# Kernel tuning notes

Measured on AMD Instinct MI355X. Metric: run time of the kernel, lower is better.

Reference implementation:

```python
import jax, jax.numpy as jnp
import numpy as np

B, S, D, H = 2, 1024, 1024, 16
DK = D // H
NEG = -1000000000.0


def setup_inputs() -> dict:
    key = jax.random.key(0)
    ks = jax.random.split(key, 12)
    def lin(kw, kb):
        # torch nn.Linear default init: U(-1/sqrt(D), 1/sqrt(D))
        bound = 1.0 / np.sqrt(D)
        W = jax.random.uniform(kw, (D, D), jnp.float32, -bound, bound)
        b = jax.random.uniform(kb, (D,), jnp.float32, -bound, bound)
        return W, b
    Wq, bq = lin(ks[0], ks[1])
    Wk, bk = lin(ks[2], ks[3])
    Wv, bv = lin(ks[4], ks[5])
    Wo, bo = lin(ks[6], ks[7])
    q = jax.random.normal(ks[8], (B, S, D), jnp.float32)
    k = jax.random.normal(ks[9], (B, S, D), jnp.float32)
    v = jax.random.normal(ks[10], (B, S, D), jnp.float32)
    mask = jnp.ones((B, 1, S), jnp.int32)  # key-padding mask, 1 = keep
    return {"q": q, "k": k, "v": v, "mask": mask,
            "Wq": Wq, "bq": bq, "Wk": Wk, "bk": bk,
            "Wv": Wv, "bv": bv, "Wo": Wo, "bo": bo}


def reference(q, k, v, mask, Wq, bq, Wk, bk, Wv, bv, Wo, bo):
    b = q.shape[0]
    # projections -> [B, H, S, DK]
    def split_heads(x):
        return x.reshape(b, -1, H, DK).transpose(0, 2, 1, 3)
    qh = split_heads(q @ Wq.T + bq)
    kh = split_heads(k @ Wk.T + bk)
    vh = split_heads(v @ Wv.T + bv)
    # scores [B, H, S, S]
    scores = jnp.einsum('bhqd,bhkd->bhqk', qh, kh) / jnp.sqrt(jnp.float32(DK))
    m = mask[:, None]  # [B,1,1,S] broadcast over heads and query dim
    scores = jnp.where(m == 0, NEG, scores)
    attn = jax.nn.softmax(scores, axis=-1)  # dropout p=0.0 -> identity
    out = jnp.einsum('bhqk,bhkd->bhqd', attn, vh)
    concat = out.transpose(0, 2, 1, 3).reshape(b, -1, D)
    return concat @ Wo.T + bo
```

## Files before the change

### kernel.cpp

```cpp
#include <hip/hip_runtime.h>

#define H 16
#define DK 64
#define SD 1024
#define DD 1024
#define BB 2
#define MROWS (BB * SD)
#define KDIM 1024

typedef __attribute__((ext_vector_type(8))) short short8;
typedef __attribute__((ext_vector_type(4))) float floatx4;
typedef unsigned short u16;
typedef __attribute__((ext_vector_type(4))) unsigned short u16x4;

#if __has_builtin(__builtin_amdgcn_exp2f)
#define EXP2(x) __builtin_amdgcn_exp2f(x)
#else
#define EXP2(x) exp2f(x)
#endif
#if __has_builtin(__builtin_amdgcn_rcpf)
#define RCP(x) __builtin_amdgcn_rcpf(x)
#else
#define RCP(x) (1.0f / (x))
#endif

__device__ __forceinline__ u16 f2bf(float f) {
    union { float f; unsigned u; } v; v.f = f;
    unsigned u = v.u;
    return (u16)((u + 0x7FFFu + ((u >> 16) & 1u)) >> 16);
}

__device__ __forceinline__ void gload16(const void* g, void* l) {
    __builtin_amdgcn_global_load_lds((const __attribute__((address_space(1))) unsigned int*)g,
                                     (__attribute__((address_space(3))) unsigned int*)l, 16, 0, 0);
}

__global__ void cvt_all(const float4* __restrict__ q, const float4* __restrict__ k,
                        const float4* __restrict__ v, const float4* __restrict__ Wq,
                        const float4* __restrict__ Wk, const float4* __restrict__ Wv,
                        const float4* __restrict__ Wo, const int* __restrict__ mask,
                        u16x4* __restrict__ qb, u16x4* __restrict__ kb, u16x4* __restrict__ vb,
                        u16x4* __restrict__ Wqb, u16x4* __restrict__ Wkb, u16x4* __restrict__ Wvb,
                        u16x4* __restrict__ Wob, float* __restrict__ maskadd) {
    const int z = blockIdx.y;
    if (z == 7) {
        const int i = blockIdx.x * blockDim.x + threadIdx.x;
        if (i < BB * SD) maskadd[i] = (mask[i] != 0) ? 0.f : -1e9f;
        return;
    }
    const float4* src; u16x4* dst; int n4;
    switch (z) {
        case 0: src = q;  dst = qb;  n4 = MROWS * DD / 4; break;
        case 1: src = k;  dst = kb;  n4 = MROWS * DD / 4; break;
        case 2: src = v;  dst = vb;  n4 = MROWS * DD / 4; break;
        case 3: src = Wq; dst = Wqb; n4 = DD * DD / 4; break;
        case 4: src = Wk; dst = Wkb; n4 = DD * DD / 4; break;
        case 5: src = Wv; dst = Wvb; n4 = DD * DD / 4; break;
        default: src = Wo; dst = Wob; n4 = DD * DD / 4; break;
    }
    for (int i = blockIdx.x * blockDim.x + threadIdx.x; i < n4; i += gridDim.x * blockDim.x) {
        float4 f = src[i];
        u16x4 o;
        o.x = f2bf(f.x); o.y = f2bf(f.y); o.z = f2bf(f.z); o.w = f2bf(f.w);
        dst[i] = o;
    }
}

__device__ __forceinline__ void gemm_main64(const u16* __restrict__ A, const u16* __restrict__ W,
                                            u16* As, u16* Bs, floatx4 (&acc)[2][4],
                                            int row0, int col0) {
    const int tid = threadIdx.x;
    const int w = tid >> 6, lane = tid & 63, lg = lane >> 4, lr = lane & 15;
    const int lrow = lane >> 3;
    const int lcol = (lane & 7) * 8;

    const u16* Abase = A + (row0 + lrow) * KDIM + lcol;
    const u16* Wbase = W + (col0 + lrow) * KDIM + lcol;

#pragma unroll
    for (int j = 0; j < 4; j++) {
        const int seg = j * 4 + w;
        gload16(Abase + seg * 8 * KDIM, As + seg * 512);
    }
#pragma unroll
    for (int j = 0; j < 2; j++) {
        const int seg = j * 4 + w;
        gload16(Wbase + seg * 8 * KDIM, Bs + seg * 512);
    }
    __syncthreads();

    int buf = 0;
    for (int k0 = 0; k0 < KDIM; k0 += 64) {
        if (k0 + 64 < KDIM) {
            const int nb = buf ^ 1;
#pragma unroll
            for (int j = 0; j < 4; j++) {
                const int seg = j * 4 + w;
                gload16(Abase + seg * 8 * KDIM + k0 + 64, As + nb * 8192 + seg * 512);
            }
#pragma unroll
            for (int j = 0; j < 2; j++) {
                const int seg = j * 4 + w;
                gload16(Wbase + seg * 8 * KDIM + k0 + 64, Bs + nb * 4096 + seg * 512);
            }
        }
        const u16* Asb = As + buf * 8192;
        const u16* Bsb = Bs + buf * 4096;
        short8 af[2][2], bf[4][2];
#pragma unroll
        for (int kk = 0; kk < 2; kk++) {
#pragma unroll
            for (int mi = 0; mi < 2; mi++)
                af[mi][kk] = *(const short8*)&Asb[(w * 32 + mi * 16 + lr) * 64 + kk * 32 + lg * 8];
#pragma unroll
            for (int ni = 0; ni < 4; ni++)
                bf[ni][kk] = *(const short8*)&Bsb[(ni * 16 + lr) * 64 + kk * 32 + lg * 8];
        }
#pragma unroll
        for (int kk = 0; kk < 2; kk++)
#pragma unroll
            for (int mi = 0; mi < 2; mi++)
#pragma unroll
                for (int ni = 0; ni < 4; ni++)
                    acc[mi][ni] = __builtin_amdgcn_mfma_f32_16x16x32_bf16(af[mi][kk], bf[ni][kk], acc[mi][ni], 0, 0, 0);
        __syncthreads();
        buf ^= 1;
    }
}

__global__ __launch_bounds__(256) void gemm_qkv(const u16* __restrict__ qb, const u16* __restrict__ kb,
                                                const u16* __restrict__ vb, const u16* __restrict__ Wqb,
                                                const u16* __restrict__ Wkb, const u16* __restrict__ Wvb,
                                                const float* __restrict__ bq, const float* __restrict__ bk,
                                                const float* __restrict__ bv,
                                                u16* __restrict__ Qh, u16* __restrict__ Kf, u16* __restrict__ Vf) {
    __shared__ u16 As[2 * 128 * 64];
    __shared__ u16 Bs[2 * 64 * 64];
    const int id = blockIdx.x;
    const int xcd = id & 7, j = id >> 3;
    const int z = j >> 5, r = j & 31;
    const int by = (xcd << 1) | (r >> 4), bx = r & 15;

    const u16 *A, *W; const float* bias; u16* out; float scale;
    if (z == 0)      { A = qb; W = Wqb; bias = bq; out = Qh; scale = 0.18033688011112042f; }
    else if (z == 1) { A = kb; W = Wkb; bias = bk; out = Kf; scale = 1.f; }
    else             { A = vb; W = Wvb; bias = bv; out = Vf; scale = 1.f; }

    const int row0 = by * 128, col0 = bx * 64;
    floatx4 acc[2][4] = {};
    gemm_main64(A, W, As, Bs, acc, row0, col0);

    const int tid = threadIdx.x;
    const int w = tid >> 6, lane = tid & 63, lg = lane >> 4, lr = lane & 15;
#pragma unroll
    for (int mi = 0; mi < 2; mi++)
#pragma unroll
        for (int ni = 0; ni < 4; ni++) {
            const int col = col0 + ni * 16 + lr;
            const float bv_ = bias[col];
            const int h = col >> 6, dk = col & 63;
#pragma unroll
            for (int rr = 0; rr < 4; rr++) {
                const int row = row0 + w * 32 + mi * 16 + lg * 4 + rr;
                const int b = row >> 10, s = row & 1023;
                const int bh = b * H + h;
                const float val = (acc[mi][ni][rr] + bv_) * scale;
                if (z == 0) {
                    out[(bh * SD + s) * DK + dk] = f2bf(val);
                } else if (z == 1) {
                    out[bh * 65536 + (s >> 4) * 1024 + (dk >> 5) * 512 +
                        ((dk >> 3) & 3) * 128 + (s & 15) * 8 + (dk & 7)] = f2bf(val);
                } else {
                    out[bh * 65536 + (s >> 6) * 4096 + ((dk >> 4) * 2 + ((s >> 5) & 1)) * 512 +
                        ((s >> 3) & 3) * 128 + (dk & 15) * 8 + (s & 7)] = f2bf(val);
                }
            }
        }
}

__global__ __launch_bounds__(256) void gemm_o(const u16* __restrict__ A, const u16* __restrict__ W,
                                              const float* __restrict__ bias, float* __restrict__ out) {
    const int id = blockIdx.x;
    const int xcd = id & 7, j = id >> 3;
    const int by = (xcd << 1) | (j >> 4), bx = j & 15;
    const int row0 = by * 128, col0 = bx * 64;
    const int tid = threadIdx.x;
    const int w = tid >> 6, lane = tid & 63, lg = lane >> 4, lr = lane & 15;

    const u16* Ar0 = A + (row0 + w * 32 + lr) * KDIM + lg * 8;
    const u16* Ar1 = A + (row0 + w * 32 + 16 + lr) * KDIM + lg * 8;
    const u16* Wr0 = W + (col0 + lr) * KDIM + lg * 8;
    const u16* Wr1 = W + (col0 + 16 + lr) * KDIM + lg * 8;
    const u16* Wr2 = W + (col0 + 32 + lr) * KDIM + lg * 8;
    const u16* Wr3 = W + (col0 + 48 + lr) * KDIM + lg * 8;

    floatx4 acc[2][4] = {};

#pragma unroll 2
    for (int k0 = 0; k0 < KDIM; k0 += 64) {
        short8 af[2][2], bf[4][2];
#pragma unroll
        for (int kk = 0; kk < 2; kk++) {
            af[0][kk] = *(const short8*)&Ar0[k0 + kk * 32];
            af[1][kk] = *(const short8*)&Ar1[k0 + kk * 32];
            bf[0][kk] = *(const short8*)&Wr0[k0 + kk * 32];
            bf[1][kk] = *(const short8*)&Wr1[k0 + kk * 32];
            bf[2][kk] = *(const short8*)&Wr2[k0 + kk * 32];
            bf[3][kk] = *(const short8*)&Wr3[k0 + kk * 32];
        }
#pragma unroll
        for (int kk = 0; kk < 2; kk++)
#pragma unroll
            for (int mi = 0; mi < 2; mi++)
#pragma unroll
                for (int ni = 0; ni < 4; ni++)
                    acc[mi][ni] = __builtin_amdgcn_mfma_f32_16x16x32_bf16(af[mi][kk], bf[ni][kk], acc[mi][ni], 0, 0, 0);
    }

#pragma unroll
    for (int mi = 0; mi < 2; mi++)
#pragma unroll
        for (int ni = 0; ni < 4; ni++) {
            const int col = col0 + ni * 16 + lr;
            const float bv_ = bias[col];
#pragma unroll
            for (int rr = 0; rr < 4; rr++) {
                const int row = row0 + w * 32 + mi * 16 + lg * 4 + rr;
                out[row * DD + col] = acc[mi][ni][rr] + bv_;
            }
        }
}

__global__ __launch_bounds__(256, 4) void attn_fused(const u16* __restrict__ Qh,
                                                     const u16* __restrict__ Kf,
                                                     const u16* __restrict__ Vf,
                                                     const float* __restrict__ maskadd,
                                                     u16* __restrict__ attn) {
    __shared__ u16 Plds[4 * 16 * 64];
    const int id = blockIdx.x;
    const int xcd = id & 7, sblk = id >> 3;
    const int bh = (xcd << 2) | (sblk >> 4);
    const int qx = sblk & 15;
    const int b = bh >> 4, h = bh & 15;
    const int tid = threadIdx.x;
    const int w = tid >> 6, lane = tid & 63;
    const int lg = lane >> 4, lr = lane & 15;
    const int q0 = qx * 64 + w * 16;

    const u16* Qb = Qh + bh * SD * DK;
    const u16* Kb = Kf + bh * 65536;
    const u16* Vb = Vf + bh * 65536;
    const float* mb = maskadd + b * SD;

    short8 aq0 = *(const short8*)&Qb[(q0 + lr) * DK + lg * 8];
    short8 aq1 = *(const short8*)&Qb[(q0 + lr) * DK + 32 + lg * 8];

    floatx4 o[4] = {};
    float lsum[4] = {0.f, 0.f, 0.f, 0.f};

    const int NIT = SD / 64;

    const int prd0 = (w << 10) | (lr << 6) | ((lg ^ (lr & 7)) << 3);
    const int prd1 = (w << 10) | (lr << 6) | (((4 + lg) ^ (lr & 7)) << 3);

    for (int it = 0; it < NIT; ++it) {
        const int kv0 = it * 64;
        const u16* Ks = Kb + kv0 * 64;
        const u16* Vs = Vb + kv0 * 64;
#pragma unroll
        for (int ct = 0; ct < 4; ct++) {
            const float ma = mb[kv0 + ct * 16 + lr];
            short8 bk0 = *(const short8*)&Ks[ct * 1024 + lg * 128 + lr * 8];
            short8 bk1 = *(const short8*)&Ks[ct * 1024 + 512 + lg * 128 + lr * 8];
            floatx4 acc = {ma, ma, ma, ma};
            acc = __builtin_amdgcn_mfma_f32_16x16x32_bf16(aq0, bk0, acc, 0, 0, 0);
            acc = __builtin_amdgcn_mfma_f32_16x16x32_bf16(aq1, bk1, acc, 0, 0, 0);
#pragma unroll
            for (int rr = 0; rr < 4; rr++) {
                const float p = EXP2(acc[rr]);
                lsum[rr] += p;
                const int row = lg * 4 + rr;
                const int slot = (ct * 2 + (lr >> 3)) ^ (row & 7);
                Plds[(w << 10) | (row << 6) | (slot << 3) | (lr & 7)] = f2bf(p);
            }
        }
        short8 pa0 = *(const short8*)&Plds[prd0];
        short8 pa1 = *(const short8*)&Plds[prd1];
#pragma unroll
        for (int cd = 0; cd < 4; cd++) {
            short8 vb0 = *(const short8*)&Vs[cd * 1024 + lg * 128 + lr * 8];
            short8 vb1 = *(const short8*)&Vs[cd * 1024 + 512 + lg * 128 + lr * 8];
            o[cd] = __builtin_amdgcn_mfma_f32_16x16x32_bf16(pa0, vb0, o[cd], 0, 0, 0);
            o[cd] = __builtin_amdgcn_mfma_f32_16x16x32_bf16(pa1, vb1, o[cd], 0, 0, 0);
        }
    }

#pragma unroll
    for (int rr = 0; rr < 4; rr++) {
        lsum[rr] += __shfl_xor(lsum[rr], 1);
        lsum[rr] += __shfl_xor(lsum[rr], 2);
        lsum[rr] += __shfl_xor(lsum[rr], 4);
        lsum[rr] += __shfl_xor(lsum[rr], 8);
    }

#pragma unroll
    for (int rr = 0; rr < 4; rr++) {
        const float inv = RCP(lsum[rr]);
        const int row = q0 + lg * 4 + rr;
#pragma unroll
        for (int cd = 0; cd < 4; cd++) {
            const int d = h * 64 + cd * 16 + lr;
            attn[(b * SD + row) * DD + d] = f2bf(o[cd][rr] * inv);
        }
    }
}

extern "C" void kernel_launch(void* const* d_in, const int* in_sizes, int n_in,
                              void* d_out, int out_size, void* d_ws, size_t ws_size,
                              hipStream_t stream) {
    const float* q  = (const float*)d_in[0];
    const float* k  = (const float*)d_in[1];
    const float* v  = (const float*)d_in[2];
    const int* mask = (const int*)d_in[3];
    const float* Wq = (const float*)d_in[4];
    const float* bq = (const float*)d_in[5];
    const float* Wk = (const float*)d_in[6];
    const float* bk = (const float*)d_in[7];
    const float* Wv = (const float*)d_in[8];
    const float* bv = (const float*)d_in[9];
    const float* Wo = (const float*)d_in[10];
    const float* bo = (const float*)d_in[11];
    float* out = (float*)d_out;

    u16* p = (u16*)d_ws;
    u16* qb  = p; p += MROWS * DD;
    u16* kb  = p; p += MROWS * DD;
    u16* vb  = p; p += MROWS * DD;
    u16* Wqb = p; p += DD * DD;
    u16* Wkb = p; p += DD * DD;
    u16* Wvb = p; p += DD * DD;
    u16* Wob = p; p += DD * DD;
    u16* Qh  = p; p += MROWS * DD;
    u16* Kf  = p; p += MROWS * DD;
    u16* Vf  = p; p += MROWS * DD;
    u16* attn = p; p += MROWS * DD;
    float* maskadd = (float*)p;

    cvt_all<<<dim3(512, 8), 256, 0, stream>>>((const float4*)q, (const float4*)k, (const float4*)v,
                                              (const float4*)Wq, (const float4*)Wk, (const float4*)Wv,
                                              (const float4*)Wo, mask,
                                              (u16x4*)qb, (u16x4*)kb, (u16x4*)vb,
                                              (u16x4*)Wqb, (u16x4*)Wkb, (u16x4*)Wvb, (u16x4*)Wob,
                                              maskadd);

    gemm_qkv<<<768, 256, 0, stream>>>(qb, kb, vb, Wqb, Wkb, Wvb, bq, bk, bv, Qh, Kf, Vf);

    attn_fused<<<512, 256, 0, stream>>>(Qh, Kf, Vf, maskadd, attn);

    gemm_o<<<256, 256, 0, stream>>>(attn, Wob, bo, out);
}
```

Measured before the change: 90.10 us.

## Store attention output and Wo in MFMA fragment-tiled layout for output GEMM

The attention kernel now writes its bf16 output, and the conversion kernel writes Wo, in a tiled layout where each 16-row by 32-k block is contiguous and matches the MFMA fragment order. The output projection GEMM then reads each lane's 16-byte fragment from a contiguous 512-element block instead of striding across 1024-element rows, which should give more coalesced global loads. The k-loop unroll also goes from 2 to 4. In exchange, the attention epilogue does scattered 2-byte stores into the tiled layout and the Wo conversion gathers from strided source rows.

```diff
diff --git a/kernel.cpp b/kernel.cpp
--- a/kernel.cpp
+++ b/kernel.cpp
@@ -34,6 +34,7 @@
     __builtin_amdgcn_global_load_lds((const __attribute__((address_space(1))) unsigned int*)g,
                                      (__attribute__((address_space(3))) unsigned int*)l, 16, 0, 0);
 }
+
 
 __global__ void cvt_all(const float4* __restrict__ q, const float4* __restrict__ k,
                         const float4* __restrict__ v, const float4* __restrict__ Wq,
@@ -48,6 +49,23 @@
         if (i < BB * SD) maskadd[i] = (mask[i] != 0) ? 0.f : -1e9f;
         return;
     }
+    if (z == 6) {
+        const int n8 = DD * DD / 8;
+        for (int i = blockIdx.x * blockDim.x + threadIdx.x; i < n8; i += gridDim.x * blockDim.x) {
+            const int t = i << 3;
+            const int s = ((t >> 14) << 4) | ((t >> 3) & 15);
+            const int kk = (((t >> 9) & 31) << 5) | (((t >> 7) & 3) << 3);
+            const int src4 = (s * DD + kk) >> 2;
+            const float4 f0 = Wo[src4];
+            const float4 f1 = Wo[src4 + 1];
+            u16x4 o0, o1;
+            o0.x = f2bf(f0.x); o0.y = f2bf(f0.y); o0.z = f2bf(f0.z); o0.w = f2bf(f0.w);
+            o1.x = f2bf(f1.x); o1.y = f2bf(f1.y); o1.z = f2bf(f1.z); o1.w = f2bf(f1.w);
+            Wob[i << 1] = o0;
+            Wob[(i << 1) | 1] = o1;
+        }
+        return;
+    }
     const float4* src; u16x4* dst; int n4;
     switch (z) {
         case 0: src = q;  dst = qb;  n4 = MROWS * DD / 4; break;
@@ -55,8 +73,7 @@
         case 2: src = v;  dst = vb;  n4 = MROWS * DD / 4; break;
         case 3: src = Wq; dst = Wqb; n4 = DD * DD / 4; break;
         case 4: src = Wk; dst = Wkb; n4 = DD * DD / 4; break;
-        case 5: src = Wv; dst = Wvb; n4 = DD * DD / 4; break;
-        default: src = Wo; dst = Wob; n4 = DD * DD / 4; break;
+        default: src = Wv; dst = Wvb; n4 = DD * DD / 4; break;
     }
     for (int i = blockIdx.x * blockDim.x + threadIdx.x; i < n4; i += gridDim.x * blockDim.x) {
         float4 f = src[i];
@@ -186,27 +203,30 @@
     const int row0 = by * 128, col0 = bx * 64;
     const int tid = threadIdx.x;
     const int w = tid >> 6, lane = tid & 63, lg = lane >> 4, lr = lane & 15;
-
-    const u16* Ar0 = A + (row0 + w * 32 + lr) * KDIM + lg * 8;
-    const u16* Ar1 = A + (row0 + w * 32 + 16 + lr) * KDIM + lg * 8;
-    const u16* Wr0 = W + (col0 + lr) * KDIM + lg * 8;
-    const u16* Wr1 = W + (col0 + 16 + lr) * KDIM + lg * 8;
-    const u16* Wr2 = W + (col0 + 32 + lr) * KDIM + lg * 8;
-    const u16* Wr3 = W + (col0 + 48 + lr) * KDIM + lg * 8;
+    const int loff = lg * 128 + lr * 8;
+
+    const u16* Af0 = A + ((row0 + w * 32) >> 4) * 16384 + loff;
+    const u16* Af1 = Af0 + 16384;
+    const u16* Wf0 = W + (col0 >> 4) * 16384 + loff;
+    const u16* Wf1 = Wf0 + 16384;
+    const u16* Wf2 = Wf0 + 2 * 16384;
+    const u16* Wf3 = Wf0 + 3 * 16384;
 
     floatx4 acc[2][4] = {};
 
-#pragma unroll 2
+#pragma unroll 4
     for (int k0 = 0; k0 < KDIM; k0 += 64) {
+        const int kb = (k0 >> 5) << 9;
         short8 af[2][2], bf[4][2];
 #pragma unroll
         for (int kk = 0; kk < 2; kk++) {
-            af[0][kk] = *(const short8*)&Ar0[k0 + kk * 32];
-            af[1][kk] = *(const short8*)&Ar1[k0 + kk * 32];
-            bf[0][kk] = *(const short8*)&Wr0[k0 + kk * 32];
-            bf[1][kk] = *(const short8*)&Wr1[k0 + kk * 32];
-            bf[2][kk] = *(const short8*)&Wr2[k0 + kk * 32];
-            bf[3][kk] = *(const short8*)&Wr3[k0 + kk * 32];
+            const int o = kb + (kk << 9);
+            af[0][kk] = *(const short8*)&Af0[o];
+            af[1][kk] = *(const short8*)&Af1[o];
+            bf[0][kk] = *(const short8*)&Wf0[o];
+            bf[1][kk] = *(const short8*)&Wf1[o];
+            bf[2][kk] = *(const short8*)&Wf2[o];
+            bf[3][kk] = *(const short8*)&Wf3[o];
         }
 #pragma unroll
         for (int kk = 0; kk < 2; kk++)
@@ -306,11 +326,12 @@
 #pragma unroll
     for (int rr = 0; rr < 4; rr++) {
         const float inv = RCP(lsum[rr]);
-        const int row = q0 + lg * 4 + rr;
+        const int s = b * SD + q0 + lg * 4 + rr;
+        const int sbase = (s >> 4) * 16384 + ((s & 15) << 3);
 #pragma unroll
         for (int cd = 0; cd < 4; cd++) {
-            const int d = h * 64 + cd * 16 + lr;
-            attn[(b * SD + row) * DD + d] = f2bf(o[cd][rr] * inv);
+            const int k = h * 64 + cd * 16 + lr;
+            attn[sbase + ((k >> 5) << 9) + (((k >> 3) & 3) << 7) + (k & 7)] = f2bf(o[cd][rr] * inv);
         }
     }
 }
```

Result: faster. 84.01 us (-6.8%).
